# Performance work log

Hardware: AMD Instinct MI355X
Metric: run time of the kernel (lower is better)

Reference implementation:

```python
import jax, jax.numpy as jnp
import numpy as np

N, C, E = 32768, 256, 16
LN_EPS = 1e-5
ENT_EPS = 1e-12


def setup_inputs() -> dict:
    key = jax.random.key(0)
    ks = jax.random.split(key, 8)
    return {
        "inputs": jax.random.normal(ks[0], (N, C), jnp.float32),
        "conv_out": jax.random.normal(ks[1], (N, C), jnp.float32),
        "domain_emb": jax.random.normal(ks[2], (C,), jnp.float32),
        "share_W": jax.random.normal(ks[3], (C, C), jnp.float32) * 0.02,
        "share_b": jnp.zeros((C,), jnp.float32),
        "gate_W": jax.random.normal(ks[4], (C, E), jnp.float32) * 0.1,
        "gate_b": jnp.zeros((E,), jnp.float32),
        "expert_W": jax.random.normal(ks[5], (E, C, C), jnp.float32) * 0.02,
        "expert_b": jnp.zeros((E, C), jnp.float32),
        "ln_gamma": jnp.ones((C,), jnp.float32),
        "ln_beta": jnp.zeros((C,), jnp.float32),
    }


def reference(inputs, conv_out, domain_emb, share_W, share_b, gate_W, gate_b,
              expert_W, expert_b, ln_gamma, ln_beta):
    n_exp = gate_W.shape[-1]

    # shared expert
    share_out = inputs @ share_W + share_b                      # (N, C)

    # LayerNorm on (stand-in) sparse-conv features + domain embedding
    mu = conv_out.mean(-1, keepdims=True)
    var = conv_out.var(-1, keepdims=True)
    route = (conv_out - mu) / jnp.sqrt(var + LN_EPS) * ln_gamma + ln_beta
    route = route + domain_emb                                   # (N, C)

    # router (eval path: no noise)
    gate_logits = route @ gate_W + gate_b                        # (N, E)
    w = jax.nn.softmax(gate_logits.astype(jnp.float32), axis=-1).astype(inputs.dtype)

    # entropy -> dynamic k per token
    entropy = -jnp.sum(w * jnp.log(w + ENT_EPS), axis=-1)        # (N,)
    max_entropy = jnp.log(jnp.float32(n_exp))
    k = jnp.ceil(1.0 + entropy / max_entropy * (n_exp - 1)).astype(jnp.int32)
    k = jnp.clip(k, 1, n_exp)                                    # (N,)

    # dynamic top-k selection mask (sort descending, keep first k)
    order = jnp.argsort(-w, axis=-1)                             # (N, E) descending ranks
    positions = jnp.arange(n_exp)[None, :]
    mask_sorted = positions < k[:, None]                         # (N, E) bool
    inv = jnp.argsort(order, axis=-1)                            # inverse permutation
    sel_mask = jnp.take_along_axis(mask_sorted, inv, axis=-1)    # (N, E) bool, expert-order
    combine = jnp.where(sel_mask, w, jnp.zeros_like(w))          # (N, E) combine weights

    # Switch-style load balancing loss
    frac_tokens = sel_mask.astype(jnp.float32).mean(0)           # (E,)
    frac_probs = w.astype(jnp.float32).mean(0)                   # (E,)
    loss_balance = jnp.mean(frac_tokens * frac_probs) * (n_exp ** 2)

    # expert compute + combine (dense, equivalent to gather/scatter loop)
    expert_out = jnp.einsum('nc,ecd->ned', inputs, expert_W) + expert_b  # (N, E, C)
    moe_out = jnp.einsum('ne,nec->nc', combine, expert_out)     # (N, C)

    return moe_out + share_out, loss_balance
```

## Files before the change

kernel.cpp:

```cpp
#include <hip/hip_runtime.h>
#include <hip/hip_bf16.h>

#define NTOK 32768
#define CH   256
#define NEXP 16

typedef __attribute__((ext_vector_type(8)))  short short8;
typedef __attribute__((ext_vector_type(16))) float f32x16;

#define MFMA32(a, b, c) __builtin_amdgcn_mfma_f32_32x32x16_bf16((a), (b), (c), 0, 0, 0)
#define BC8(v) __builtin_bit_cast(short8, (v))

#define GLD16(lds, g) __builtin_amdgcn_global_load_lds(                          \
    (const __attribute__((address_space(1))) unsigned int*)(g),                  \
    (__attribute__((address_space(3))) unsigned int*)(lds), 16, 0, 0)

static __device__ __forceinline__ unsigned short f2bf(float f) {
  unsigned int u = __builtin_bit_cast(unsigned int, f);
  unsigned int r = (u + 0x7fffu + ((u >> 16) & 1u)) >> 16;
  return (unsigned short)r;
}


__global__ __launch_bounds__(256) void wconvert_kernel(
    const float* __restrict__ share_W, const float* __restrict__ expert_W,
    uint4* __restrict__ wp) {
  int g = blockIdx.x * 256 + threadIdx.x;
  int e = g >> 13;
  int r = g & 8191;
  int lane = r & 63;
  int kb = (r >> 6) & 15;
  int db = r >> 10;
  int d  = db * 32 + (lane & 31);
  int k0 = kb * 16 + ((lane >> 5) << 3);
  const float* src = (e < 16) ? (expert_W + (size_t)e * 65536) : share_W;
  unsigned int p[4];
#pragma unroll
  for (int j = 0; j < 4; j++) {
    float f0 = src[(size_t)(k0 + 2 * j) * 256 + d];
    float f1 = src[(size_t)(k0 + 2 * j + 1) * 256 + d];
    p[j] = (unsigned int)f2bf(f0) | ((unsigned int)f2bf(f1) << 16);
  }
  wp[g] = make_uint4(p[0], p[1], p[2], p[3]);
}

__global__ __launch_bounds__(512, 2) void gate_kernel(
    const float* __restrict__ inputs, const float* __restrict__ conv_out,
    const float* __restrict__ domain_emb, const float* __restrict__ gate_W,
    const float* __restrict__ gate_b, const float* __restrict__ ln_gamma,
    const float* __restrict__ ln_beta, uint4* __restrict__ apack,
    float* __restrict__ combine, float* __restrict__ frac_part) {
  __shared__ __align__(16) unsigned short atile[64 * 256];
  __shared__ __align__(16) float gwT[16 * 260];
  __shared__ float route[8][256];
  __shared__ float fred[2][8][16];
  int t = threadIdx.x, b = blockIdx.x;
  int w = t >> 6, l = t & 63;

  for (int i = 0; i < 8; i++) {
    int idx = i * 512 + t;
    gwT[(idx & 15) * 260 + (idx >> 4)] = gate_W[idx];
  }

  for (int i = 0; i < 4; i++) {
    int idx = i * 512 + t;
    int row = idx >> 5;
    int j = idx & 31;
    const float4* src = (const float4*)(inputs + ((size_t)b * 64 + row) * 256 + j * 8);
    float4 f0 = src[0], f1 = src[1];
    unsigned int p0 = (unsigned int)f2bf(f0.x) | ((unsigned int)f2bf(f0.y) << 16);
    unsigned int p1 = (unsigned int)f2bf(f0.z) | ((unsigned int)f2bf(f0.w) << 16);
    unsigned int p2 = (unsigned int)f2bf(f1.x) | ((unsigned int)f2bf(f1.y) << 16);
    unsigned int p3 = (unsigned int)f2bf(f1.z) | ((unsigned int)f2bf(f1.w) << 16);
    int s = j ^ (row & 31);
    *(uint4*)(atile + (row * 32 + s) * 8) = make_uint4(p0, p1, p2, p3);
  }
  __syncthreads();
  for (int i = 0; i < 4; i++) {
    int L = i * 512 + t;
    int ll = L & 63;
    int mb = (L >> 6) & 1, kb = L >> 7;
    int row = mb * 32 + (ll & 31);
    int j = kb * 2 + (ll >> 5);
    int s = j ^ (row & 31);
    apack[(size_t)b * 2048 + L] = *(const uint4*)(atile + (row * 32 + s) * 8);
  }

  int lc = l * 4;
  float4 g4 = *(const float4*)(ln_gamma + lc);
  float4 be4 = *(const float4*)(ln_beta + lc);
  float4 de4 = *(const float4*)(domain_emb + lc);
  int e = l & 15, q = l >> 4;
  float gb = gate_b[e];
  float psel = 0.f, pw = 0.f;

  float4 gwreg[16];
#pragma unroll
  for (int ii = 0; ii < 16; ii++)
    gwreg[ii] = *(const float4*)&gwT[e * 260 + q * 64 + ii * 4];

  int n0 = b * 64 + w * 8;
  float4 x = *(const float4*)(conv_out + (size_t)n0 * 256 + lc);
  for (int i = 0; i < 8; i++) {
    float4 xn = *(const float4*)(conv_out + (size_t)(n0 + ((i + 1) & 7)) * 256 + lc);

    float s1 = x.x + x.y + x.z + x.w;
#pragma unroll
    for (int off = 1; off < 64; off <<= 1) s1 += __shfl_xor(s1, off);
    float mu = s1 * (1.f / 256.f);
    float dx = x.x - mu, dy = x.y - mu, dz = x.z - mu, dw = x.w - mu;
    float s2 = dx * dx + dy * dy + dz * dz + dw * dw;
#pragma unroll
    for (int off = 1; off < 64; off <<= 1) s2 += __shfl_xor(s2, off);
    float rstd = rsqrtf(s2 * (1.f / 256.f) + 1e-5f);
    float4 r;
    r.x = dx * rstd * g4.x + be4.x + de4.x;
    r.y = dy * rstd * g4.y + be4.y + de4.y;
    r.z = dz * rstd * g4.z + be4.z + de4.z;
    r.w = dw * rstd * g4.w + be4.w + de4.w;
    *(float4*)(&route[w][lc]) = r;
    asm volatile("s_waitcnt lgkmcnt(0)" ::: "memory");
    __builtin_amdgcn_wave_barrier();

    float a0 = 0.f, a1 = 0.f, a2 = 0.f, a3 = 0.f;
#pragma unroll
    for (int ii = 0; ii < 16; ii += 4) {
      float4 r0 = *(const float4*)(&route[w][q * 64 + (ii + 0) * 4]);
      float4 r1 = *(const float4*)(&route[w][q * 64 + (ii + 1) * 4]);
      float4 r2 = *(const float4*)(&route[w][q * 64 + (ii + 2) * 4]);
      float4 r3 = *(const float4*)(&route[w][q * 64 + (ii + 3) * 4]);
      a0 += r0.x * gwreg[ii + 0].x + r0.y * gwreg[ii + 0].y + r0.z * gwreg[ii + 0].z + r0.w * gwreg[ii + 0].w;
      a1 += r1.x * gwreg[ii + 1].x + r1.y * gwreg[ii + 1].y + r1.z * gwreg[ii + 1].z + r1.w * gwreg[ii + 1].w;
      a2 += r2.x * gwreg[ii + 2].x + r2.y * gwreg[ii + 2].y + r2.z * gwreg[ii + 2].z + r2.w * gwreg[ii + 2].w;
      a3 += r3.x * gwreg[ii + 3].x + r3.y * gwreg[ii + 3].y + r3.z * gwreg[ii + 3].z + r3.w * gwreg[ii + 3].w;
    }
    float acc = (a0 + a1) + (a2 + a3);
    acc += __shfl_xor(acc, 16);
    acc += __shfl_xor(acc, 32);
    float logit = acc + gb;

    float m = logit;
#pragma unroll
    for (int off = 1; off < 16; off <<= 1) m = fmaxf(m, __shfl_xor(m, off));
    float p = expf(logit - m);
    float sum = p;
#pragma unroll
    for (int off = 1; off < 16; off <<= 1) sum += __shfl_xor(sum, off);
    float wv = p / sum;

    float et = -wv * logf(wv + 1e-12f);
    float ent = et;
#pragma unroll
    for (int off = 1; off < 16; off <<= 1) ent += __shfl_xor(ent, off);
    float kf = ceilf(1.f + ent * (15.f / 2.7725887f));
    int k = (int)kf;
    k = max(1, min(16, k));

    int base = l & 48;
    int rank = 0;
#pragma unroll
    for (int j = 0; j < 16; j++) {
      float wj = __shfl(wv, base + j);
      rank += (wj > wv) || (wj == wv && j < e);
    }
    int sel = rank < k;
    float cmb = sel ? wv : 0.f;
    int n = n0 + i;
    if (l < 16) combine[(size_t)n * 16 + e] = cmb;
    psel += (float)sel;
    pw += wv;

    x = xn;
  }

  if (l < 16) { fred[0][w][l] = psel; fred[1][w][l] = pw; }
  __syncthreads();
  if (t < 32) {
    int kind = t >> 4, ee = t & 15;
    float v = 0.f;
#pragma unroll
    for (int ww = 0; ww < 8; ww++) v += fred[kind][ww][ee];
    frac_part[b * 32 + t] = v;
  }
}

__global__ __launch_bounds__(512, 2) void moe_gemm_kernel(
    const uint4* __restrict__ apack, const uint4* __restrict__ wpack,
    const float* __restrict__ combine, const float* __restrict__ expert_b,
    const float* __restrict__ share_b, float* __restrict__ out) {
  extern __shared__ __align__(16) char smem[];
  uint4* atile  = (uint4*)smem;
  uint4* btile0 = (uint4*)(smem + 65536);
  uint4* btile1 = (uint4*)(smem + 98304);
  float* wtile  = (float*)(smem + 131072);

  int t = threadIdx.x, b = blockIdx.x;
  int w = t >> 6, l = t & 63;
  int mbp = w >> 2;
  int dbp = w & 3;

#pragma unroll
  for (int i = 0; i < 8; i++) {
    int g = w * 8 + i;
    int kb = g >> 2, mb = g & 3;
    const uint4* src = apack + ((size_t)(2 * b + (mb >> 1)) * 2048 + (size_t)(kb * 2 + (mb & 1)) * 64 + l);
    GLD16(atile + g * 64, src);
  }
#pragma unroll
  for (int i = 0; i < 4; i++) {
    int g = w * 4 + i;
    int kbl = g >> 3, db = g & 7;
    GLD16(btile0 + g * 64, wpack + ((size_t)db * 1024 + kbl * 64 + l));
  }
  {
    const float* cg = combine + (size_t)b * 2048;
#pragma unroll
    for (int i = 0; i < 4; i++) {
      int idx = i * 512 + t;
      wtile[(idx & 15) * 128 + (idx >> 4)] = cg[idx];
    }
  }
  asm volatile("s_waitcnt lgkmcnt(0)" ::: "memory");

  f32x16 facc[2][2];
#pragma unroll
  for (int mi = 0; mi < 2; mi++)
#pragma unroll
    for (int d = 0; d < 2; d++)
#pragma unroll
      for (int r = 0; r < 16; r++) facc[mi][d][r] = 0.f;
  f32x16 zc;
#pragma unroll
  for (int r = 0; r < 16; r++) zc[r] = 0.f;

  short8 areg[2][4];
  f32x16 tacc[2][2];
  uint4* bufs[2] = {btile0, btile1};
  int rowoff = (l >> 5) * 4;

  for (int e = 0; e < 17; e++) {
#pragma unroll
    for (int q = 0; q < 4; q++) {
      int s = e * 4 + q;

      asm volatile("" ::: "memory");
      __builtin_amdgcn_s_barrier();

      if (s < 67) {
        int sn = s + 1;
        int en = sn >> 2, qn = sn & 3;
        uint4* nb = bufs[sn & 1];
#pragma unroll
        for (int i = 0; i < 4; i++) {
          int g = w * 4 + i;
          int kbl = g >> 3, db = g & 7;
          GLD16(nb + g * 64,
                wpack + ((size_t)en * 8192 + (size_t)db * 1024 + (qn * 4 + kbl) * 64 + l));
        }
        asm volatile("s_waitcnt vmcnt(4)" ::: "memory");
      } else {
        asm volatile("s_waitcnt vmcnt(0)" ::: "memory");
      }

      __builtin_amdgcn_s_barrier();
      asm volatile("" ::: "memory");

#pragma unroll
      for (int mi = 0; mi < 2; mi++)
#pragma unroll
        for (int kbl = 0; kbl < 4; kbl++)
          areg[mi][kbl] = BC8(atile[((size_t)(q * 4 + kbl) * 4 + (mbp * 2 + mi)) * 64 + l]);

      const uint4* cb = bufs[s & 1];
      __builtin_amdgcn_s_setprio(1);
      if (q == 0) {
        {
          short8 b0 = BC8(cb[(size_t)(0 * 8 + dbp * 2 + 0) * 64 + l]);
          short8 b1 = BC8(cb[(size_t)(0 * 8 + dbp * 2 + 1) * 64 + l]);
          tacc[0][0] = MFMA32(areg[0][0], b0, zc);
          tacc[0][1] = MFMA32(areg[0][0], b1, zc);
          tacc[1][0] = MFMA32(areg[1][0], b0, zc);
          tacc[1][1] = MFMA32(areg[1][0], b1, zc);
        }
#pragma unroll
        for (int kbl = 1; kbl < 4; kbl++) {
          short8 b0 = BC8(cb[(size_t)(kbl * 8 + dbp * 2 + 0) * 64 + l]);
          short8 b1 = BC8(cb[(size_t)(kbl * 8 + dbp * 2 + 1) * 64 + l]);
          tacc[0][0] = MFMA32(areg[0][kbl], b0, tacc[0][0]);
          tacc[0][1] = MFMA32(areg[0][kbl], b1, tacc[0][1]);
          tacc[1][0] = MFMA32(areg[1][kbl], b0, tacc[1][0]);
          tacc[1][1] = MFMA32(areg[1][kbl], b1, tacc[1][1]);
        }
      } else {
#pragma unroll
        for (int kbl = 0; kbl < 4; kbl++) {
          short8 b0 = BC8(cb[(size_t)(kbl * 8 + dbp * 2 + 0) * 64 + l]);
          short8 b1 = BC8(cb[(size_t)(kbl * 8 + dbp * 2 + 1) * 64 + l]);
          tacc[0][0] = MFMA32(areg[0][kbl], b0, tacc[0][0]);
          tacc[0][1] = MFMA32(areg[0][kbl], b1, tacc[0][1]);
          tacc[1][0] = MFMA32(areg[1][kbl], b0, tacc[1][0]);
          tacc[1][1] = MFMA32(areg[1][kbl], b1, tacc[1][1]);
        }
      }
      __builtin_amdgcn_s_setprio(0);

      if (q == 3) {
        if (e < 16) {
#pragma unroll
          for (int mi = 0; mi < 2; mi++)
#pragma unroll
            for (int rg = 0; rg < 4; rg++) {
              float4 w4 = *(const float4*)&wtile[e * 128 + (mbp * 2 + mi) * 32 + 8 * rg + rowoff];
              float wj[4] = {w4.x, w4.y, w4.z, w4.w};
#pragma unroll
              for (int j = 0; j < 4; j++) {
                facc[mi][0][rg * 4 + j] += wj[j] * tacc[mi][0][rg * 4 + j];
                facc[mi][1][rg * 4 + j] += wj[j] * tacc[mi][1][rg * 4 + j];
              }
            }
        } else {
#pragma unroll
          for (int mi = 0; mi < 2; mi++)
#pragma unroll
            for (int r = 0; r < 16; r++) {
              facc[mi][0][r] += tacc[mi][0][r];
              facc[mi][1][r] += tacc[mi][1][r];
            }
        }
      }
    }
  }

  int col = l & 31;
  int cg0 = (dbp * 2 + 0) * 32 + col;
  int cg1 = (dbp * 2 + 1) * 32 + col;
  float sb0 = share_b[cg0], sb1 = share_b[cg1];
  float eb0[16], eb1[16];
#pragma unroll
  for (int e2 = 0; e2 < 16; e2++) {
    eb0[e2] = expert_b[e2 * 256 + cg0];
    eb1[e2] = expert_b[e2 * 256 + cg1];
  }
#pragma unroll
  for (int e2 = 0; e2 < 16; e2++)
#pragma unroll
    for (int mi = 0; mi < 2; mi++)
#pragma unroll
      for (int rg = 0; rg < 4; rg++) {
        float4 w4 = *(const float4*)&wtile[e2 * 128 + (mbp * 2 + mi) * 32 + 8 * rg + rowoff];
        float wj[4] = {w4.x, w4.y, w4.z, w4.w};
#pragma unroll
        for (int j = 0; j < 4; j++) {
          facc[mi][0][rg * 4 + j] += wj[j] * eb0[e2];
          facc[mi][1][rg * 4 + j] += wj[j] * eb1[e2];
        }
      }
#pragma unroll
  for (int mi = 0; mi < 2; mi++)
#pragma unroll
    for (int r = 0; r < 16; r++) {
      int row = (mbp * 2 + mi) * 32 + (r & 3) + ((r >> 2) << 3) + rowoff;
      size_t n = (size_t)b * 128 + row;
      out[n * 256 + cg0] = facc[mi][0][r] + sb0;
      out[n * 256 + cg1] = facc[mi][1][r] + sb1;
    }
}

__global__ __launch_bounds__(256) void finalize_kernel(
    const float* __restrict__ frac_part, float* __restrict__ loss_out) {
  __shared__ float acc[8][32];
  int t = threadIdx.x;
  int col = t & 31, seg = t >> 5;
  float s = 0.f;
  for (int i = seg; i < 512; i += 8) s += frac_part[i * 32 + col];
  acc[seg][col] = s;
  __syncthreads();
  if (t < 32) {
    float v = 0.f;
#pragma unroll
    for (int sg = 0; sg < 8; sg++) v += acc[sg][t];
    acc[0][t] = v;
  }
  __syncthreads();
  if (t == 0) {
    float loss = 0.f;
    for (int e = 0; e < 16; e++) {
      float ft = acc[0][e] * (1.f / 32768.f);
      float fp = acc[0][16 + e] * (1.f / 32768.f);
      loss += ft * fp;
    }
    loss_out[0] = loss * 16.f;
  }
}

extern "C" void kernel_launch(void* const* d_in, const int* in_sizes, int n_in,
                              void* d_out, int out_size, void* d_ws, size_t ws_size,
                              hipStream_t stream) {
  const float* inputs   = (const float*)d_in[0];
  const float* conv_out = (const float*)d_in[1];
  const float* demb     = (const float*)d_in[2];
  const float* share_W  = (const float*)d_in[3];
  const float* share_b  = (const float*)d_in[4];
  const float* gate_W   = (const float*)d_in[5];
  const float* gate_b   = (const float*)d_in[6];
  const float* expert_W = (const float*)d_in[7];
  const float* expert_b = (const float*)d_in[8];
  const float* ln_g     = (const float*)d_in[9];
  const float* ln_b     = (const float*)d_in[10];
  float* out = (float*)d_out;
  char* ws = (char*)d_ws;

  uint4* apack   = (uint4*)(ws);
  uint4* wpack   = (uint4*)(ws + 16777216);
  float* combine = (float*)(ws + 19005440);
  float* frac    = (float*)(ws + 21102592);

  hipFuncSetAttribute((const void*)moe_gemm_kernel,
                      hipFuncAttributeMaxDynamicSharedMemorySize, 139264);

  wconvert_kernel<<<dim3(544), dim3(256), 0, stream>>>(share_W, expert_W, wpack);
  gate_kernel<<<dim3(512), dim3(512), 0, stream>>>(inputs, conv_out, demb, gate_W,
                                                   gate_b, ln_g, ln_b, apack, combine, frac);
  moe_gemm_kernel<<<dim3(256), dim3(512), 139264, stream>>>(apack, wpack, combine,
                                                            expert_b, share_b, out);
  finalize_kernel<<<dim3(1), dim3(256), 0, stream>>>(frac, out + 8388608);
}
```

Baseline: 244.6 us.

## Load expert weights directly into registers with software prefetch, drop LDS B tiles

The MoE GEMM kernel no longer stages expert weight tiles through double-buffered LDS with per-slot barriers. Each wave now loads its own B fragments straight from global memory into registers, prefetching one k-slot ahead in alternating register sets, and reads A fragments from LDS inline. This removes two barriers per k-slot and shrinks dynamic LDS from 139264 to 73728 bytes. In exchange, B data shared across waves is now fetched from global/L2 redundantly by each wave, and register pressure rises.

```diff
diff --git a/kernel.cpp b/kernel.cpp
--- a/kernel.cpp
+++ b/kernel.cpp
@@ -184,15 +184,47 @@
   }
 }
 
+static __device__ __forceinline__ void pref_b(
+    uint4 (&breg)[8], const uint4* __restrict__ we, int q) {
+#pragma unroll
+  for (int f = 0; f < 8; f++) {
+    int kbl = f >> 1, d = f & 1;
+    breg[f] = we[(size_t)d * 1024 + (q * 4 + kbl) * 64];
+  }
+}
+
+static __device__ __forceinline__ void slot_mfma(
+    f32x16 (&tacc)[2][2], const f32x16& zc, const uint4* __restrict__ ab,
+    const uint4 (&breg)[8], int q, bool first) {
+  __builtin_amdgcn_s_setprio(1);
+#pragma unroll
+  for (int kbl = 0; kbl < 4; kbl++) {
+    short8 a0 = BC8(ab[(q * 4 + kbl) * 256]);
+    short8 a1 = BC8(ab[(q * 4 + kbl) * 256 + 64]);
+    short8 b0 = BC8(breg[kbl * 2 + 0]);
+    short8 b1 = BC8(breg[kbl * 2 + 1]);
+    if (first && kbl == 0) {
+      tacc[0][0] = MFMA32(a0, b0, zc);
+      tacc[0][1] = MFMA32(a0, b1, zc);
+      tacc[1][0] = MFMA32(a1, b0, zc);
+      tacc[1][1] = MFMA32(a1, b1, zc);
+    } else {
+      tacc[0][0] = MFMA32(a0, b0, tacc[0][0]);
+      tacc[0][1] = MFMA32(a0, b1, tacc[0][1]);
+      tacc[1][0] = MFMA32(a1, b0, tacc[1][0]);
+      tacc[1][1] = MFMA32(a1, b1, tacc[1][1]);
+    }
+  }
+  __builtin_amdgcn_s_setprio(0);
+}
+
 __global__ __launch_bounds__(512, 2) void moe_gemm_kernel(
     const uint4* __restrict__ apack, const uint4* __restrict__ wpack,
     const float* __restrict__ combine, const float* __restrict__ expert_b,
     const float* __restrict__ share_b, float* __restrict__ out) {
   extern __shared__ __align__(16) char smem[];
-  uint4* atile  = (uint4*)smem;
-  uint4* btile0 = (uint4*)(smem + 65536);
-  uint4* btile1 = (uint4*)(smem + 98304);
-  float* wtile  = (float*)(smem + 131072);
+  uint4* atile = (uint4*)smem;
+  float* wtile = (float*)(smem + 65536);
 
   int t = threadIdx.x, b = blockIdx.x;
   int w = t >> 6, l = t & 63;
@@ -206,12 +238,6 @@
     const uint4* src = apack + ((size_t)(2 * b + (mb >> 1)) * 2048 + (size_t)(kb * 2 + (mb & 1)) * 64 + l);
     GLD16(atile + g * 64, src);
   }
-#pragma unroll
-  for (int i = 0; i < 4; i++) {
-    int g = w * 4 + i;
-    int kbl = g >> 3, db = g & 7;
-    GLD16(btile0 + g * 64, wpack + ((size_t)db * 1024 + kbl * 64 + l));
-  }
   {
     const float* cg = combine + (size_t)b * 2048;
 #pragma unroll
@@ -220,7 +246,7 @@
       wtile[(idx & 15) * 128 + (idx >> 4)] = cg[idx];
     }
   }
-  asm volatile("s_waitcnt lgkmcnt(0)" ::: "memory");
+  __syncthreads();
 
   f32x16 facc[2][2];
 #pragma unroll
@@ -233,101 +259,47 @@
 #pragma unroll
   for (int r = 0; r < 16; r++) zc[r] = 0.f;
 
-  short8 areg[2][4];
   f32x16 tacc[2][2];
-  uint4* bufs[2] = {btile0, btile1};
   int rowoff = (l >> 5) * 4;
 
+  const uint4* ab = atile + (size_t)(mbp * 2) * 64 + l;
+  const uint4* wb = wpack + (size_t)(dbp * 2) * 1024 + l;
+
+  uint4 bregA[8], bregB[8];
+  pref_b(bregA, wb, 0);
+
   for (int e = 0; e < 17; e++) {
-#pragma unroll
-    for (int q = 0; q < 4; q++) {
-      int s = e * 4 + q;
-
-      asm volatile("" ::: "memory");
-      __builtin_amdgcn_s_barrier();
-
-      if (s < 67) {
-        int sn = s + 1;
-        int en = sn >> 2, qn = sn & 3;
-        uint4* nb = bufs[sn & 1];
-#pragma unroll
-        for (int i = 0; i < 4; i++) {
-          int g = w * 4 + i;
-          int kbl = g >> 3, db = g & 7;
-          GLD16(nb + g * 64,
-                wpack + ((size_t)en * 8192 + (size_t)db * 1024 + (qn * 4 + kbl) * 64 + l));
+    const uint4* we = wb + (size_t)e * 8192;
+    pref_b(bregB, we, 1);
+    slot_mfma(tacc, zc, ab, bregA, 0, true);
+    pref_b(bregA, we, 2);
+    slot_mfma(tacc, zc, ab, bregB, 1, false);
+    pref_b(bregB, we, 3);
+    slot_mfma(tacc, zc, ab, bregA, 2, false);
+    if (e < 16) pref_b(bregA, we + 8192, 0);
+    slot_mfma(tacc, zc, ab, bregB, 3, false);
+
+    if (e < 16) {
+#pragma unroll
+      for (int mi = 0; mi < 2; mi++)
+#pragma unroll
+        for (int rg = 0; rg < 4; rg++) {
+          float4 w4 = *(const float4*)&wtile[e * 128 + (mbp * 2 + mi) * 32 + 8 * rg + rowoff];
+          float wj[4] = {w4.x, w4.y, w4.z, w4.w};
+#pragma unroll
+          for (int j = 0; j < 4; j++) {
+            facc[mi][0][rg * 4 + j] += wj[j] * tacc[mi][0][rg * 4 + j];
+            facc[mi][1][rg * 4 + j] += wj[j] * tacc[mi][1][rg * 4 + j];
+          }
         }
-        asm volatile("s_waitcnt vmcnt(4)" ::: "memory");
-      } else {
-        asm volatile("s_waitcnt vmcnt(0)" ::: "memory");
-      }
-
-      __builtin_amdgcn_s_barrier();
-      asm volatile("" ::: "memory");
-
+    } else {
 #pragma unroll
       for (int mi = 0; mi < 2; mi++)
 #pragma unroll
-        for (int kbl = 0; kbl < 4; kbl++)
-          areg[mi][kbl] = BC8(atile[((size_t)(q * 4 + kbl) * 4 + (mbp * 2 + mi)) * 64 + l]);
-
-      const uint4* cb = bufs[s & 1];
-      __builtin_amdgcn_s_setprio(1);
-      if (q == 0) {
-        {
-          short8 b0 = BC8(cb[(size_t)(0 * 8 + dbp * 2 + 0) * 64 + l]);
-          short8 b1 = BC8(cb[(size_t)(0 * 8 + dbp * 2 + 1) * 64 + l]);
-          tacc[0][0] = MFMA32(areg[0][0], b0, zc);
-          tacc[0][1] = MFMA32(areg[0][0], b1, zc);
-          tacc[1][0] = MFMA32(areg[1][0], b0, zc);
-          tacc[1][1] = MFMA32(areg[1][0], b1, zc);
+        for (int r = 0; r < 16; r++) {
+          facc[mi][0][r] += tacc[mi][0][r];
+          facc[mi][1][r] += tacc[mi][1][r];
         }
-#pragma unroll
-        for (int kbl = 1; kbl < 4; kbl++) {
-          short8 b0 = BC8(cb[(size_t)(kbl * 8 + dbp * 2 + 0) * 64 + l]);
-          short8 b1 = BC8(cb[(size_t)(kbl * 8 + dbp * 2 + 1) * 64 + l]);
-          tacc[0][0] = MFMA32(areg[0][kbl], b0, tacc[0][0]);
-          tacc[0][1] = MFMA32(areg[0][kbl], b1, tacc[0][1]);
-          tacc[1][0] = MFMA32(areg[1][kbl], b0, tacc[1][0]);
-          tacc[1][1] = MFMA32(areg[1][kbl], b1, tacc[1][1]);
-        }
-      } else {
-#pragma unroll
-        for (int kbl = 0; kbl < 4; kbl++) {
-          short8 b0 = BC8(cb[(size_t)(kbl * 8 + dbp * 2 + 0) * 64 + l]);
-          short8 b1 = BC8(cb[(size_t)(kbl * 8 + dbp * 2 + 1) * 64 + l]);
-          tacc[0][0] = MFMA32(areg[0][kbl], b0, tacc[0][0]);
-          tacc[0][1] = MFMA32(areg[0][kbl], b1, tacc[0][1]);
-          tacc[1][0] = MFMA32(areg[1][kbl], b0, tacc[1][0]);
-          tacc[1][1] = MFMA32(areg[1][kbl], b1, tacc[1][1]);
-        }
-      }
-      __builtin_amdgcn_s_setprio(0);
-
-      if (q == 3) {
-        if (e < 16) {
-#pragma unroll
-          for (int mi = 0; mi < 2; mi++)
-#pragma unroll
-            for (int rg = 0; rg < 4; rg++) {
-              float4 w4 = *(const float4*)&wtile[e * 128 + (mbp * 2 + mi) * 32 + 8 * rg + rowoff];
-              float wj[4] = {w4.x, w4.y, w4.z, w4.w};
-#pragma unroll
-              for (int j = 0; j < 4; j++) {
-                facc[mi][0][rg * 4 + j] += wj[j] * tacc[mi][0][rg * 4 + j];
-                facc[mi][1][rg * 4 + j] += wj[j] * tacc[mi][1][rg * 4 + j];
-              }
-            }
-        } else {
-#pragma unroll
-          for (int mi = 0; mi < 2; mi++)
-#pragma unroll
-            for (int r = 0; r < 16; r++) {
-              facc[mi][0][r] += tacc[mi][0][r];
-              facc[mi][1][r] += tacc[mi][1][r];
-            }
-        }
-      }
     }
   }
 
@@ -416,12 +388,12 @@
   float* frac    = (float*)(ws + 21102592);
 
   hipFuncSetAttribute((const void*)moe_gemm_kernel,
-                      hipFuncAttributeMaxDynamicSharedMemorySize, 139264);
+                      hipFuncAttributeMaxDynamicSharedMemorySize, 73728);
 
   wconvert_kernel<<<dim3(544), dim3(256), 0, stream>>>(share_W, expert_W, wpack);
   gate_kernel<<<dim3(512), dim3(512), 0, stream>>>(inputs, conv_out, demb, gate_W,
                                                    gate_b, ln_g, ln_b, apack, combine, frac);
-  moe_gemm_kernel<<<dim3(256), dim3(512), 139264, stream>>>(apack, wpack, combine,
-                                                            expert_b, share_b, out);
+  moe_gemm_kernel<<<dim3(256), dim3(512), 73728, stream>>>(apack, wpack, combine,
+                                                           expert_b, share_b, out);
   finalize_kernel<<<dim3(1), dim3(256), 0, stream>>>(frac, out + 8388608);
 }
```

Result: no change. 241.0 us (-1.5%).
